# Kernel tuning notes

Measured on AMD Instinct MI355X. Metric: run time of the kernel, lower is better.

The kernel has to match this reference:

```python
import jax, jax.numpy as jnp
import numpy as np

NOISE_STD = 0.01  # noise_std init arg


def setup_inputs() -> dict:
    key = jax.random.key(0)
    k1, k2, k3, k4, k5 = jax.random.split(key, 5)
    B, C, H, W = 32, 256, 56, 56
    x = jax.random.normal(k1, (B, C, H, W), dtype=jnp.float32)
    H_real = jax.random.normal(k2, (B, C, C), dtype=jnp.float32)
    H_imag = jax.random.normal(k3, (B, C, C), dtype=jnp.float32)
    noise_real = jax.random.normal(k4, (B, C, H, W), dtype=jnp.float32)
    noise_imag = jax.random.normal(k5, (B, C, H, W), dtype=jnp.float32)
    return {"x": x, "H_real": H_real, "H_imag": H_imag,
            "noise_real": noise_real, "noise_imag": noise_imag}


def reference(x, H_real, H_imag, noise_real, noise_imag):
    # x: (B,C,H,W) real. Per-batch complex MIMO channel Hc = (Hr + i*Hi)/sqrt(2*C).
    # Since x has zero imaginary part, y = Hc @ x splits into two real GEMMs.
    C = x.shape[1]
    scale = 1.0 / jnp.sqrt(jnp.asarray(2.0 * C, dtype=x.dtype))
    yr = jnp.einsum('bij,bjhw->bihw', H_real, x) * scale + noise_real * NOISE_STD
    yi = jnp.einsum('bij,bjhw->bihw', H_imag, x) * scale + noise_imag * NOISE_STD
    # output_mode == 'magnitude' -> |y|
    return jnp.sqrt(yr * yr + yi * yi)
```

## Files before the change

### kernel.cpp

```cpp
#include <hip/hip_runtime.h>
#include <hip/hip_bf16.h>
#include <math.h>


#define NBATCH 32
#define NC 256
#define NP 3136
#define BM 128
#define BN 64
#define BK 32
#define NBN 49
#define NKI 8

typedef __attribute__((ext_vector_type(8))) short short8;
typedef __attribute__((ext_vector_type(4))) float f32x4;

static __device__ __forceinline__ void gload16(const void* g, void* l) {
  __builtin_amdgcn_global_load_lds(
      (const __attribute__((address_space(1))) void*)g,
      (__attribute__((address_space(3))) void*)l, 16, 0, 0);
}

static __device__ __forceinline__ unsigned short bfr(float f) {
  __hip_bfloat16 h = __float2bfloat16(f);
  return *reinterpret_cast<unsigned short*>(&h);
}

__global__ __launch_bounds__(256)
void perm_h_kernel(const float* __restrict__ hr, const float* __restrict__ hi,
                   unsigned short* __restrict__ ws)
{
  const int blk   = blockIdx.x;
  const int kt    = blk & 7;
  const int b2m   = blk >> 3;
  const int plane = threadIdx.x >> 7;
  const int row   = threadIdx.x & 127;
  const int b     = b2m >> 1;
  const int bm    = b2m & 1;

  const float* src = (plane ? hi : hr)
      + ((size_t)b * NC + bm * 128 + row) * NC + kt * 32;
  unsigned short* dst = ws + ((size_t)(b2m * 8 + kt) * 2 + plane) * 4096 + row * 8;

  #pragma unroll
  for (int fq = 0; fq < 4; ++fq) {
    const float4 v0 = *reinterpret_cast<const float4*>(src + fq * 8);
    const float4 v1 = *reinterpret_cast<const float4*>(src + fq * 8 + 4);
    union { uint4 v; unsigned short u[8]; } o;
    o.u[0] = bfr(v0.x); o.u[1] = bfr(v0.y); o.u[2] = bfr(v0.z); o.u[3] = bfr(v0.w);
    o.u[4] = bfr(v1.x); o.u[5] = bfr(v1.y); o.u[6] = bfr(v1.z); o.u[7] = bfr(v1.w);
    *reinterpret_cast<uint4*>(dst + fq * 1024) = o.v;
  }
}

template<int PRE>
__global__ __launch_bounds__(512, 6)
void rayleigh_main(const float* __restrict__ xg,
                   const float* __restrict__ Hrg,
                   const float* __restrict__ Hig,
                   const unsigned short* __restrict__ Hperm,
                   const float* __restrict__ nrg,
                   const float* __restrict__ nig,
                   float* __restrict__ outg)
{
  __shared__ float x_lds[2][BK * BN];
  __shared__ unsigned short hr_lds[2][4096];
  __shared__ unsigned short hi_lds[2][4096];

  const int raw = blockIdx.x;
  const int v   = (raw & 7) * 392 + (raw >> 3);
  const int b   = v / 98;
  const int r2  = v - b * 98;
  const int bm  = r2 / 49;
  const int bn  = r2 - bm * 49;

  const int tid  = threadIdx.x;
  const int lane = tid & 63;
  const int wave = tid >> 6;
  const int wm   = wave >> 2;
  const int wn   = wave & 3;
  const int fr   = lane & 15;
  const int fq   = lane >> 4;

  const float* xsrc = xg + (size_t)b * NC * NP + (size_t)bn * BN;
  const size_t hrowbase = (size_t)b * NC + bm * BM;
  const size_t hpbase   = (size_t)((b * 2 + bm) * 8);

  auto stage = [&](int t, int buf) {
    {
      const int C16 = wave * 64 + lane;
      const int k   = C16 >> 4;
      const int cp  = C16 & 15;
      const int fqk = k >> 3;
      const int cl  = cp ^ (((fqk & 1) << 2) | (fqk >> 1));
      const float* src = xsrc + (size_t)(t * BK + k) * NP + cl * 4;
      gload16(src, (char*)x_lds[buf] + wave * 1024);
    }
    if constexpr (PRE) {
      #pragma unroll
      for (int i = 0; i < 2; ++i) {
        const int c     = wave * 2 + i;
        const int plane = c >> 3;
        const int fqc   = (c >> 1) & 3;
        const int half  = c & 1;
        unsigned short* hl = plane ? hi_lds[buf] : hr_lds[buf];
        const unsigned short* src = Hperm
            + ((hpbase + t) * 2 + plane) * 4096
            + fqc * 1024 + (half * 64 + lane) * 8;
        gload16(src, (char*)hl + fqc * 2048 + half * 1024);
      }
    }
  };

  f32x4 accR[4], accI[4];
  #pragma unroll
  for (int m = 0; m < 4; ++m) {
    accR[m] = (f32x4){0.f, 0.f, 0.f, 0.f};
    accI[m] = (f32x4){0.f, 0.f, 0.f, 0.f};
  }

  const int xork = ((fq & 1) << 6) | ((fq >> 1) << 4);
  const int pcol = ((wn * 16 + fr) << 2) ^ xork;

  stage(0, 0);

  #pragma unroll
  for (int t = 0; t < NKI; ++t) {
    __syncthreads();
    if (t + 1 < NKI) stage(t + 1, (t + 1) & 1);

    const char* xbuf = (const char*)x_lds[t & 1];
    union { short8 s; unsigned short u[8]; } u;
    #pragma unroll
    for (int j = 0; j < 8; ++j) {
      const float f = *reinterpret_cast<const float*>(xbuf + ((fq * 8 + j) << 8) + pcol);
      u.u[j] = bfr(f);
    }
    const short8 xb = u.s;

    #pragma unroll
    for (int m = 0; m < 4; ++m) {
      const int row = wm * 64 + m * 16 + fr;
      short8 ar, ai;
      if constexpr (PRE) {
        ar = *reinterpret_cast<const short8*>(&hr_lds[t & 1][fq * 1024 + row * 8]);
        ai = *reinterpret_cast<const short8*>(&hi_lds[t & 1][fq * 1024 + row * 8]);
      } else {
        const float* p1 = Hrg + (hrowbase + row) * NC + t * 32 + fq * 8;
        const float* p2 = Hig + (hrowbase + row) * NC + t * 32 + fq * 8;
        const float4 v0 = *reinterpret_cast<const float4*>(p1);
        const float4 v1 = *reinterpret_cast<const float4*>(p1 + 4);
        const float4 w0 = *reinterpret_cast<const float4*>(p2);
        const float4 w1 = *reinterpret_cast<const float4*>(p2 + 4);
        union { short8 s; unsigned short uu[8]; } a1, a2;
        a1.uu[0] = bfr(v0.x); a1.uu[1] = bfr(v0.y); a1.uu[2] = bfr(v0.z); a1.uu[3] = bfr(v0.w);
        a1.uu[4] = bfr(v1.x); a1.uu[5] = bfr(v1.y); a1.uu[6] = bfr(v1.z); a1.uu[7] = bfr(v1.w);
        a2.uu[0] = bfr(w0.x); a2.uu[1] = bfr(w0.y); a2.uu[2] = bfr(w0.z); a2.uu[3] = bfr(w0.w);
        a2.uu[4] = bfr(w1.x); a2.uu[5] = bfr(w1.y); a2.uu[6] = bfr(w1.z); a2.uu[7] = bfr(w1.w);
        ar = a1.s; ai = a2.s;
      }
      accR[m] = __builtin_amdgcn_mfma_f32_16x16x32_bf16(xb, ar, accR[m], 0, 0, 0);
      accI[m] = __builtin_amdgcn_mfma_f32_16x16x32_bf16(xb, ai, accI[m], 0, 0, 0);
    }
  }

  const float scale = 0.04419417382415922f;
  const float nstd  = 0.01f;
  const size_t obase = ((size_t)b * NC + bm * BM + wm * 64 + fr) * NP
                     + (size_t)bn * BN + wn * 16 + fq * 4;
  #pragma unroll
  for (int m = 0; m < 4; ++m) {
    const size_t idx = obase + (size_t)(m * 16) * NP;
    const float4 nr4 = *reinterpret_cast<const float4*>(nrg + idx);
    const float4 ni4 = *reinterpret_cast<const float4*>(nig + idx);
    float4 o;
    {
      const float yr = accR[m][0] * scale + nr4.x * nstd;
      const float yi = accI[m][0] * scale + ni4.x * nstd;
      o.x = sqrtf(yr * yr + yi * yi);
    }
    {
      const float yr = accR[m][1] * scale + nr4.y * nstd;
      const float yi = accI[m][1] * scale + ni4.y * nstd;
      o.y = sqrtf(yr * yr + yi * yi);
    }
    {
      const float yr = accR[m][2] * scale + nr4.z * nstd;
      const float yi = accI[m][2] * scale + ni4.z * nstd;
      o.z = sqrtf(yr * yr + yi * yi);
    }
    {
      const float yr = accR[m][3] * scale + nr4.w * nstd;
      const float yi = accI[m][3] * scale + ni4.w * nstd;
      o.w = sqrtf(yr * yr + yi * yi);
    }
    *reinterpret_cast<float4*>(outg + idx) = o;
  }
}

extern "C" void kernel_launch(void* const* d_in, const int* in_sizes, int n_in,
                              void* d_out, int out_size, void* d_ws, size_t ws_size,
                              hipStream_t stream) {
  const float* x  = (const float*)d_in[0];
  const float* Hr = (const float*)d_in[1];
  const float* Hi = (const float*)d_in[2];
  const float* nr = (const float*)d_in[3];
  const float* ni = (const float*)d_in[4];
  float* out = (float*)d_out;

  const size_t HN = (size_t)NBATCH * NC * NC;

  if (ws_size >= HN * 2 * sizeof(unsigned short)) {
    unsigned short* hperm = (unsigned short*)d_ws;
    hipLaunchKernelGGL(perm_h_kernel, dim3(512), dim3(256), 0, stream, Hr, Hi, hperm);
    hipLaunchKernelGGL((rayleigh_main<1>), dim3(NBATCH * 2 * NBN), dim3(512), 0, stream,
                       x, Hr, Hi, hperm, nr, ni, out);
  } else {
    hipLaunchKernelGGL((rayleigh_main<0>), dim3(NBATCH * 2 * NBN), dim3(512), 0, stream,
                       x, Hr, Hi, (const unsigned short*)nullptr, nr, ni, out);
  }
}
```

Baseline: 116.4 us.

## Prefetch noise tiles inside the K loop and relax the per-iteration barrier wait

The noise_real and noise_imag loads move out of the epilogue and are issued one per K iteration, so they overlap with the MFMA main loop instead of stalling at the end. In the precomputed-H path, __syncthreads is replaced by an explicit s_waitcnt vmcnt(1) plus s_barrier, so the newest noise load can stay in flight across the barrier. The launch-bounds occupancy hint drops from 6 to 4 blocks, which allows more registers for the eight prefetched float4 values but may lower occupancy. The hand-counted vmcnt relies on in-order completion of global_load_lds and normal loads.

```diff
diff --git a/kernel.cpp b/kernel.cpp
--- a/kernel.cpp
+++ b/kernel.cpp
@@ -54,7 +54,7 @@
 }
 
 template<int PRE>
-__global__ __launch_bounds__(512, 6)
+__global__ __launch_bounds__(512, 4)
 void rayleigh_main(const float* __restrict__ xg,
                    const float* __restrict__ Hrg,
                    const float* __restrict__ Hig,
@@ -118,7 +118,10 @@
     accR[m] = (f32x4){0.f, 0.f, 0.f, 0.f};
     accI[m] = (f32x4){0.f, 0.f, 0.f, 0.f};
   }
-
+  float4 nrv4[4], niv4[4];
+
+  const size_t obase = ((size_t)b * NC + bm * BM + wm * 64 + fr) * NP
+                     + (size_t)bn * BN + wn * 16 + fq * 4;
   const int xork = ((fq & 1) << 6) | ((fq >> 1) << 4);
   const int pcol = ((wn * 16 + fr) << 2) ^ xork;
 
@@ -126,8 +129,22 @@
 
   #pragma unroll
   for (int t = 0; t < NKI; ++t) {
-    __syncthreads();
+    if constexpr (PRE) {
+      if (t == 0) asm volatile("s_waitcnt vmcnt(0)" ::: "memory");
+      else        asm volatile("s_waitcnt vmcnt(1)" ::: "memory");
+      __builtin_amdgcn_s_barrier();
+      __builtin_amdgcn_sched_barrier(0);
+    } else {
+      __syncthreads();
+    }
     if (t + 1 < NKI) stage(t + 1, (t + 1) & 1);
+
+    {
+      const int m = t >> 1;
+      const size_t nidx = obase + (size_t)(m * 16) * NP;
+      if ((t & 1) == 0) nrv4[m] = *reinterpret_cast<const float4*>(nrg + nidx);
+      else              niv4[m] = *reinterpret_cast<const float4*>(nig + nidx);
+    }
 
     const char* xbuf = (const char*)x_lds[t & 1];
     union { short8 s; unsigned short u[8]; } u;
@@ -166,32 +183,28 @@
 
   const float scale = 0.04419417382415922f;
   const float nstd  = 0.01f;
-  const size_t obase = ((size_t)b * NC + bm * BM + wm * 64 + fr) * NP
-                     + (size_t)bn * BN + wn * 16 + fq * 4;
   #pragma unroll
   for (int m = 0; m < 4; ++m) {
     const size_t idx = obase + (size_t)(m * 16) * NP;
-    const float4 nr4 = *reinterpret_cast<const float4*>(nrg + idx);
-    const float4 ni4 = *reinterpret_cast<const float4*>(nig + idx);
     float4 o;
     {
-      const float yr = accR[m][0] * scale + nr4.x * nstd;
-      const float yi = accI[m][0] * scale + ni4.x * nstd;
+      const float yr = accR[m][0] * scale + nrv4[m].x * nstd;
+      const float yi = accI[m][0] * scale + niv4[m].x * nstd;
       o.x = sqrtf(yr * yr + yi * yi);
     }
     {
-      const float yr = accR[m][1] * scale + nr4.y * nstd;
-      const float yi = accI[m][1] * scale + ni4.y * nstd;
+      const float yr = accR[m][1] * scale + nrv4[m].y * nstd;
+      const float yi = accI[m][1] * scale + niv4[m].y * nstd;
       o.y = sqrtf(yr * yr + yi * yi);
     }
     {
-      const float yr = accR[m][2] * scale + nr4.z * nstd;
-      const float yi = accI[m][2] * scale + ni4.z * nstd;
+      const float yr = accR[m][2] * scale + nrv4[m].z * nstd;
+      const float yi = accI[m][2] * scale + niv4[m].z * nstd;
       o.z = sqrtf(yr * yr + yi * yi);
     }
     {
-      const float yr = accR[m][3] * scale + nr4.w * nstd;
-      const float yi = accI[m][3] * scale + ni4.w * nstd;
+      const float yr = accR[m][3] * scale + nrv4[m].w * nstd;
+      const float yi = accI[m][3] * scale + niv4[m].w * nstd;
       o.w = sqrtf(yr * yr + yi * yi);
     }
     *reinterpret_cast<float4*>(outg + idx) = o;
```

After: 120.3 us. +3.4%, slower.
